# Kernel tuning notes

Hardware: AMD Instinct MI355X
Metric: run time of the kernel (lower is better)

Reference implementation:

```python
import jax, jax.numpy as jnp
import numpy as np

D = 64        # input_dim == hidden dims
D2 = 2 * D    # transformer model dim
N = 20000     # num_nodes
R = 24        # num_relation
S = 3         # history snapshots
E = 60000     # edges per snapshot
B = 8         # batch
K = 101       # candidates (1 pos + 100 neg)
HLEN = 50     # history length
NL_GNN = 2
NL_TF = 2
NH = 2        # attention heads
HD = D2 // NH


def setup_inputs() -> dict:
    key = jax.random.key(0)
    ks = list(jax.random.split(key, 40))
    nrm = lambda i, shape: jax.random.normal(ks[i], shape, jnp.float32) * 0.05
    inp = {}
    # embeddings / params
    inp["poi_emb"] = nrm(0, (N, D))
    inp["query_emb"] = nrm(1, (R, D))
    inp["gate_W"] = nrm(2, (D, D)); inp["gate_b"] = jnp.zeros((D,), jnp.float32)
    inp["gnn_rel"] = nrm(3, (NL_GNN, R, D))
    inp["gnn_W"] = nrm(4, (NL_GNN, 2 * D, D)); inp["gnn_b"] = jnp.zeros((NL_GNN, D), jnp.float32)
    inp["g_time_emb"] = nrm(5, (48, D))
    inp["g_lin_W"] = nrm(6, (D, D)); inp["g_lin_b"] = jnp.zeros((D,), jnp.float32)
    inp["tf_Wqkv"] = nrm(7, (NL_TF, D2, 3 * D2))
    inp["tf_Wo"] = nrm(8, (NL_TF, D2, D2))
    ln = jnp.stack([jnp.ones((NL_TF, D2), jnp.float32), jnp.zeros((NL_TF, D2), jnp.float32)], axis=1)
    inp["tf_ln1"] = ln; inp["tf_ln2"] = ln
    inp["tf_W1"] = nrm(9, (NL_TF, D2, 4 * D2)); inp["tf_b1"] = jnp.zeros((NL_TF, 4 * D2), jnp.float32)
    inp["tf_W2"] = nrm(10, (NL_TF, 4 * D2, D2)); inp["tf_b2"] = jnp.zeros((NL_TF, D2), jnp.float32)
    F_DIM = D + D2  # hidden_dims[-1] + 2*input_dim
    inp["mlp_W1"] = nrm(11, (F_DIM, F_DIM)); inp["mlp_b1"] = jnp.zeros((F_DIM,), jnp.float32)
    inp["mlp_W2"] = nrm(12, (F_DIM, 1)); inp["mlp_b2"] = jnp.zeros((1,), jnp.float32)
    inp["history_time_encoding"] = nrm(13, (B, HLEN, D2))
    # graph / index inputs
    inp["edge_src"] = jax.random.randint(ks[14], (S, E), 0, N)
    inp["edge_dst"] = jax.random.randint(ks[15], (S, E), 0, N)
    inp["edge_type"] = jax.random.randint(ks[16], (S, E), 0, R)
    inp["h_index"] = jax.random.randint(ks[17], (B,), 0, N)
    inp["r_index"] = jax.random.randint(ks[18], (B,), 0, R)
    inp["t_index"] = jax.random.randint(ks[19], (B, K), 0, N)
    inp["history_poi"] = jax.random.randint(ks[20], (B, HLEN), 0, N)
    inp["g_time"] = jax.random.randint(ks[21], (S,), 0, 48)
    return inp


def _layer_norm(x, scale, bias):
    m = x.mean(-1, keepdims=True)
    v = ((x - m) ** 2).mean(-1, keepdims=True)
    return (x - m) * jax.lax.rsqrt(v + 1e-5) * scale + bias


def reference(poi_emb, query_emb, gate_W, gate_b, gnn_rel, gnn_W, gnn_b,
              g_time_emb, g_lin_W, g_lin_b,
              tf_Wqkv, tf_Wo, tf_ln1, tf_W1, tf_b1, tf_W2, tf_b2, tf_ln2,
              mlp_W1, mlp_b1, mlp_W2, mlp_b2,
              history_time_encoding,
              edge_src, edge_dst, edge_type, h_index, r_index, t_index,
              history_poi, g_time):
    query = query_emb[r_index]  # [B, D]  (r_index constant across candidates)
    output = jnp.zeros((B, N, D), poi_emb.dtype)
    for s in range(S):  # temporal snapshot loop (memory_update per snapshot)
        src, dst, et = edge_src[s], edge_dst[s], edge_type[s]
        # scatter_add of poi embeddings over both endpoints; identical per batch row
        poi_node = jnp.concatenate([src, dst])  # [2E]
        init_one = jax.ops.segment_sum(poi_emb[poi_node], poi_node, num_segments=N)  # [N, D]
        init = jnp.broadcast_to(init_one[None], (B, N, D))
        if s > 0:
            gate = jax.nn.sigmoid(output @ gate_W + gate_b)  # sigmoid gating vs prior state
            init = init * gate + (1.0 - gate) * output
        x = init
        for l in range(NL_GNN):  # PathAggNet stack: transe message + scatter-sum + linear
            msg = x[:, src] + gnn_rel[l][et][None]  # [B, E, D]
            agg = jnp.zeros((B, N, D), x.dtype).at[:, dst].add(msg)  # [B, N, D]
            x = jax.nn.relu(jnp.concatenate([agg, init], axis=-1) @ gnn_W[l] + gnn_b[l])
        output = x
        query = (query + g_time_emb[g_time[s]][None]) @ g_lin_W + g_lin_b
    feature = output  # [B, N, D]
    r_emb = jnp.broadcast_to(query[:, None], (B, N, D))
    final_feature = jnp.concatenate([feature, r_emb], axis=-1)  # [B, N, 2D]
    # gather history POI features + time encoding -> transformer encoder
    poi_idx = jnp.broadcast_to(history_poi[..., None], (B, HLEN, D2))
    xseq = jnp.take_along_axis(final_feature, poi_idx, axis=1) + history_time_encoding  # [B, HLEN, 2D]
    for l in range(NL_TF):
        qkv = xseq @ tf_Wqkv[l]  # [B, HLEN, 3*D2]
        q, k, v = jnp.split(qkv, 3, axis=-1)
        split_heads = lambda t: t.reshape(B, HLEN, NH, HD).transpose(0, 2, 1, 3)
        q, k, v = split_heads(q), split_heads(k), split_heads(v)
        att = jax.nn.softmax(jnp.einsum('bnqd,bnkd->bnqk', q, k) / jnp.sqrt(jnp.float32(HD)), axis=-1)
        o = jnp.einsum('bnqk,bnkd->bnqd', att, v).transpose(0, 2, 1, 3).reshape(B, HLEN, D2) @ tf_Wo[l]
        xseq = _layer_norm(xseq + o, tf_ln1[l, 0], tf_ln1[l, 1])
        ff = jax.nn.relu(xseq @ tf_W1[l] + tf_b1[l]) @ tf_W2[l] + tf_b2[l]
        xseq = _layer_norm(xseq + ff, tf_ln2[l, 0], tf_ln2[l, 1])
    feature_label = xseq.mean(axis=1, keepdims=True)  # [B, 1, 2D]
    t_idx = jnp.broadcast_to(t_index[..., None], (B, K, D))
    feature_t = jnp.take_along_axis(feature, t_idx, axis=1)  # [B, K, D]
    feature_t = jnp.concatenate([feature_t, jnp.broadcast_to(feature_label, (B, K, D2))], axis=-1)
    hmid = jax.nn.relu(feature_t @ mlp_W1 + mlp_b1)
    score = (hmid @ mlp_W2 + mlp_b2).squeeze(-1)  # [B, K]
    return score
```

## Files before the change

### kernel.cpp

```cpp
#include <hip/hip_runtime.h>
#include <hip/hip_bf16.h>
#include <math.h>

#define DD   64
#define DD2  128
#define NN   20000
#define RR   24
#define SS   3
#define EE   60000
#define BB   8
#define KK   101
#define HLENN 50
#define MROWS 20024

__global__ void hist_kernel(const int* __restrict__ src, const int* __restrict__ dst,
                            int* __restrict__ hist, int* __restrict__ deg) {
    int s = blockIdx.y;
    int e = blockIdx.x * 256 + threadIdx.x;
    if (e < EE) {
        int d0 = dst[s * EE + e], s0 = src[s * EE + e];
        atomicAdd(&hist[s * NN + d0], 1);
        atomicAdd(&deg[s * NN + d0], 1);
        atomicAdd(&deg[s * NN + s0], 1);
    }
}

__global__ void scan_kernel(const int* __restrict__ hist, int* __restrict__ rowptr,
                            int* __restrict__ cursor) {
    int s = blockIdx.x, t = threadIdx.x;
    const int* h = hist + s * NN;
    int* rp = rowptr + s * (NN + 1);
    int* cur = cursor + s * NN;
    __shared__ int sp[1024];
    int base = t * 20, sum = 0;
    for (int i = 0; i < 20; ++i) { int idx = base + i; if (idx < NN) sum += h[idx]; }
    sp[t] = sum;
    __syncthreads();
    for (int off = 1; off < 1024; off <<= 1) {
        int v = (t >= off) ? sp[t - off] : 0;
        __syncthreads();
        sp[t] += v;
        __syncthreads();
    }
    int run = sp[t] - sum;
    for (int i = 0; i < 20; ++i) {
        int idx = base + i;
        if (idx < NN) { rp[idx] = run; cur[idx] = run; run += h[idx]; }
    }
    if (t == 1023) rp[NN] = sp[1023];
}

__global__ void place_kernel(const int* __restrict__ src, const int* __restrict__ dst,
                             const int* __restrict__ et, int* __restrict__ cursor,
                             int* __restrict__ colp) {
    int s = blockIdx.y;
    int e = blockIdx.x * 256 + threadIdx.x;
    if (e < EE) {
        int d0 = dst[s * EE + e];
        int pos = atomicAdd(&cursor[s * NN + d0], 1);
        colp[s * EE + pos] = src[s * EE + e] | (et[s * EE + e] << 16);
    }
}

__global__ void init_kernel(const float* __restrict__ poi, const int* __restrict__ deg,
                            const float* __restrict__ gate_W, const float* __restrict__ gate_b,
                            const float* __restrict__ xprev, float* __restrict__ initb,
                            int use_gate) {
    __shared__ float sW[64][64];
    __shared__ float srow[4][64];
    int li = threadIdx.x >> 6, d = threadIdx.x & 63;
    int node = blockIdx.x * 4 + li;
    if (use_gate) {
        for (int i = threadIdx.x; i < 64 * 64; i += 256) sW[i >> 6][i & 63] = gate_W[i];
    }
    float iv = (float)deg[node] * poi[node * 64 + d];
    if (use_gate) {
        float ov = xprev[node * 64 + d];
        srow[li][d] = ov;
        __syncthreads();
        float acc = gate_b[d];
        #pragma unroll
        for (int k = 0; k < 64; ++k) acc += srow[li][k] * sW[k][d];
        float g = 1.f / (1.f + expf(-acc));
        iv = iv * g + (1.f - g) * ov;
    }
    initb[node * 64 + d] = iv;
}

__global__ void gemm64_kernel(const float* __restrict__ A0a, const float* __restrict__ Ar_a,
                              const float* __restrict__ Ba, float* __restrict__ Ca,
                              const float* __restrict__ A0b, const float* __restrict__ Ar_b,
                              const float* __restrict__ Bb, float* __restrict__ Cb) {
    const float* A0 = blockIdx.y ? A0b : A0a;
    const float* Ar = blockIdx.y ? Ar_b : Ar_a;
    const float* B  = blockIdx.y ? Bb  : Ba;
    float* C        = blockIdx.y ? Cb  : Ca;
    __shared__ float sA[64][68];
    __shared__ float sB[64][68];
    int tid = threadIdx.x;
    int row0 = blockIdx.x * 64;
    for (int i = tid; i < 64 * 16; i += 256) {
        int r = i >> 4, cq = i & 15;
        int row = row0 + r;
        float4 v = make_float4(0.f, 0.f, 0.f, 0.f);
        if (row < NN)        v = *(const float4*)(A0 + (size_t)row * 64 + cq * 4);
        else if (row < MROWS) v = *(const float4*)(Ar + (size_t)(row - NN) * 64 + cq * 4);
        *(float4*)&sA[r][cq * 4] = v;
        if (i < 64 * 16) {
            float4 w = *(const float4*)(B + (size_t)r * 64 + cq * 4);
            *(float4*)&sB[r][cq * 4] = w;
        }
    }
    __syncthreads();
    int tr = tid >> 4, tc = tid & 15;
    float acc[4][4] = {{0.f}};
    #pragma unroll 16
    for (int k = 0; k < 64; ++k) {
        float4 b4 = *(const float4*)&sB[k][tc * 4];
        float a0 = sA[tr * 4 + 0][k];
        float a1 = sA[tr * 4 + 1][k];
        float a2 = sA[tr * 4 + 2][k];
        float a3 = sA[tr * 4 + 3][k];
        acc[0][0] += a0 * b4.x; acc[0][1] += a0 * b4.y; acc[0][2] += a0 * b4.z; acc[0][3] += a0 * b4.w;
        acc[1][0] += a1 * b4.x; acc[1][1] += a1 * b4.y; acc[1][2] += a1 * b4.z; acc[1][3] += a1 * b4.w;
        acc[2][0] += a2 * b4.x; acc[2][1] += a2 * b4.y; acc[2][2] += a2 * b4.z; acc[2][3] += a2 * b4.w;
        acc[3][0] += a3 * b4.x; acc[3][1] += a3 * b4.y; acc[3][2] += a3 * b4.z; acc[3][3] += a3 * b4.w;
    }
    #pragma unroll
    for (int i = 0; i < 4; ++i) {
        int row = row0 + tr * 4 + i;
        if (row < MROWS) {
            float4 o = make_float4(acc[i][0], acc[i][1], acc[i][2], acc[i][3]);
            *(float4*)(C + (size_t)row * 64 + tc * 4) = o;
        }
    }
}

__global__ void fin_kernel(const float* __restrict__ y, const float* __restrict__ z,
                           const int* __restrict__ rowptr, const int* __restrict__ colp,
                           const float* __restrict__ bias, float* __restrict__ xout) {
    __shared__ float srelW[24][64];
    int tid = threadIdx.x;
    for (int i = tid; i < 24 * 64; i += 256) srelW[i >> 6][i & 63] = y[NN * 64 + i];
    int d = tid & 63, w = tid >> 6;
    float bb = bias[d];
    __syncthreads();
    int base = blockIdx.x * 16 + w * 4;
    for (int n = 0; n < 4; ++n) {
        int node = base + n;
        float acc = z[node * 64 + d] + bb;
        int e0 = rowptr[node], e1 = rowptr[node + 1];
        for (int e = e0; e < e1; ++e) {
            int pack = colp[e];
            acc += y[(size_t)(pack & 0xFFFF) * 64 + d] + srelW[pack >> 16][d];
        }
        xout[node * 64 + d] = fmaxf(acc, 0.f);
    }
}

__global__ void query_kernel(const float* __restrict__ query_emb, const int* __restrict__ r_index,
                             const float* __restrict__ g_time_emb, const int* __restrict__ g_time,
                             const float* __restrict__ g_lin_W, const float* __restrict__ g_lin_b,
                             float* __restrict__ query) {
    __shared__ float sW[64][64];
    __shared__ float sq[8][64];
    int b = threadIdx.x >> 6;
    int d = threadIdx.x & 63;
    for (int i = threadIdx.x; i < 64 * 64; i += 512) sW[i >> 6][i & 63] = g_lin_W[i];
    float q = query_emb[r_index[b] * 64 + d];
    for (int s = 0; s < SS; ++s) {
        float t = q + g_time_emb[g_time[s] * 64 + d];
        sq[b][d] = t;
        __syncthreads();
        float acc = g_lin_b[d];
        #pragma unroll
        for (int k = 0; k < 64; ++k) acc += sq[b][k] * sW[k][d];
        q = acc;
        __syncthreads();
    }
    query[b * 64 + d] = q;
}

__global__ void xseq_kernel(const float* __restrict__ feature, const float* __restrict__ query,
                            const int* __restrict__ history_poi, const float* __restrict__ hte,
                            float* __restrict__ xseq) {
    int idx = blockIdx.x * 256 + threadIdx.x;
    if (idx >= BB * HLENN * DD2) return;
    int c = idx & 127;
    int bt = idx >> 7;
    int b = bt / HLENN, t = bt % HLENN;
    float v = (c < 64) ? feature[history_poi[b * HLENN + t] * 64 + c]
                       : query[b * 64 + (c - 64)];
    xseq[idx] = v + hte[idx];
}

__global__ void qkv4_kernel(const float* __restrict__ xseq, const float* __restrict__ Wqkv,
                            float* __restrict__ qkvb) {
    __shared__ float sx[4][128];
    int tid = threadIdx.x;
    int row0 = blockIdx.x * 4;
    for (int i = tid; i < 512; i += 384) sx[i >> 7][i & 127] = xseq[row0 * 128 + i];
    __syncthreads();
    float a0 = 0.f, a1 = 0.f, a2 = 0.f, a3 = 0.f;
    #pragma unroll 8
    for (int k = 0; k < 128; ++k) {
        float w = Wqkv[k * 384 + tid];
        a0 += sx[0][k] * w; a1 += sx[1][k] * w; a2 += sx[2][k] * w; a3 += sx[3][k] * w;
    }
    qkvb[(row0 + 0) * 384 + tid] = a0;
    qkvb[(row0 + 1) * 384 + tid] = a1;
    qkvb[(row0 + 2) * 384 + tid] = a2;
    qkvb[(row0 + 3) * 384 + tid] = a3;
}

__global__ void attn_kernel(const float* __restrict__ qkv, float* __restrict__ attnout) {
    int b = blockIdx.x >> 1, h = blockIdx.x & 1;
    __shared__ float sq[HLENN][64], sk[HLENN][64], sv[HLENN][64];
    __shared__ float ss[HLENN][HLENN];
    for (int i = threadIdx.x; i < HLENN * 64; i += 256) {
        int t = i >> 6, d = i & 63;
        const float* base = qkv + (size_t)(b * HLENN + t) * 384 + h * 64 + d;
        sq[t][d] = base[0];
        sk[t][d] = base[128];
        sv[t][d] = base[256];
    }
    __syncthreads();
    for (int p = threadIdx.x; p < HLENN * HLENN; p += 256) {
        int i = p / HLENN, j = p % HLENN;
        float acc = 0.f;
        #pragma unroll 8
        for (int d = 0; d < 64; ++d) acc += sq[i][d] * sk[j][d];
        ss[i][j] = acc * 0.125f;
    }
    __syncthreads();
    if (threadIdx.x < HLENN) {
        int i = threadIdx.x;
        float m = -1e30f;
        for (int j = 0; j < HLENN; ++j) m = fmaxf(m, ss[i][j]);
        float sum = 0.f;
        for (int j = 0; j < HLENN; ++j) { float e = expf(ss[i][j] - m); ss[i][j] = e; sum += e; }
        float inv = 1.f / sum;
        for (int j = 0; j < HLENN; ++j) ss[i][j] *= inv;
    }
    __syncthreads();
    for (int p = threadIdx.x; p < HLENN * 64; p += 256) {
        int i = p >> 6, d = p & 63;
        float acc = 0.f;
        for (int j = 0; j < HLENN; ++j) acc += ss[i][j] * sv[j][d];
        attnout[(size_t)(b * HLENN + i) * 128 + h * 64 + d] = acc;
    }
}

__global__ void addLN4_kernel(const float* __restrict__ aout, const float* __restrict__ Wo,
                              const float* __restrict__ ln, float* __restrict__ xseq) {
    __shared__ float sa[4][128];
    __shared__ float sred[4][128];
    int tid = threadIdx.x;
    int r = tid >> 7, c = tid & 127;
    int row0 = blockIdx.x * 4;
    sa[r][c] = aout[(row0 + r) * 128 + c];
    __syncthreads();
    float acc = xseq[(row0 + r) * 128 + c];
    #pragma unroll 8
    for (int k = 0; k < 128; ++k) acc += sa[r][k] * Wo[k * 128 + c];
    sred[r][c] = acc; __syncthreads();
    for (int off = 64; off > 0; off >>= 1) { if (c < off) sred[r][c] += sred[r][c + off]; __syncthreads(); }
    float mean = sred[r][0] * (1.f / 128.f);
    __syncthreads();
    float dx = acc - mean;
    sred[r][c] = dx * dx; __syncthreads();
    for (int off = 64; off > 0; off >>= 1) { if (c < off) sred[r][c] += sred[r][c + off]; __syncthreads(); }
    float var = sred[r][0] * (1.f / 128.f);
    xseq[(row0 + r) * 128 + c] = dx * rsqrtf(var + 1e-5f) * ln[c] + ln[128 + c];
}

__global__ void ffLN4_kernel(const float* __restrict__ xin, const float* __restrict__ W1,
                             const float* __restrict__ b1, const float* __restrict__ W2,
                             const float* __restrict__ b2, const float* __restrict__ ln,
                             float* __restrict__ xout) {
    __shared__ float sx[4][128];
    __shared__ float sh[4][512];
    __shared__ float spart[4][4][128];
    __shared__ float sred[4][128];
    int tid = threadIdx.x;
    int row0 = blockIdx.x * 4;
    { int r = tid >> 7, c = tid & 127; sx[r][c] = xin[(row0 + r) * 128 + c]; }
    __syncthreads();
    {
        float bb = b1[tid];
        float a0 = bb, a1 = bb, a2 = bb, a3 = bb;
        #pragma unroll 8
        for (int k = 0; k < 128; ++k) {
            float w = W1[k * 512 + tid];
            a0 += sx[0][k] * w; a1 += sx[1][k] * w; a2 += sx[2][k] * w; a3 += sx[3][k] * w;
        }
        sh[0][tid] = fmaxf(a0, 0.f); sh[1][tid] = fmaxf(a1, 0.f);
        sh[2][tid] = fmaxf(a2, 0.f); sh[3][tid] = fmaxf(a3, 0.f);
    }
    __syncthreads();
    int kc = tid >> 7, c = tid & 127;
    float p0 = 0.f, p1 = 0.f, p2 = 0.f, p3 = 0.f;
    #pragma unroll 8
    for (int kk = 0; kk < 128; ++kk) {
        int k = kc * 128 + kk;
        float w = W2[k * 128 + c];
        p0 += sh[0][k] * w; p1 += sh[1][k] * w; p2 += sh[2][k] * w; p3 += sh[3][k] * w;
    }
    spart[kc][0][c] = p0; spart[kc][1][c] = p1; spart[kc][2][c] = p2; spart[kc][3][c] = p3;
    __syncthreads();
    int r = kc;
    float acc = b2[c] + spart[0][r][c] + spart[1][r][c] + spart[2][r][c] + spart[3][r][c] + sx[r][c];
    sred[r][c] = acc; __syncthreads();
    for (int off = 64; off > 0; off >>= 1) { if (c < off) sred[r][c] += sred[r][c + off]; __syncthreads(); }
    float mean = sred[r][0] * (1.f / 128.f);
    __syncthreads();
    float dx = acc - mean;
    sred[r][c] = dx * dx; __syncthreads();
    for (int off = 64; off > 0; off >>= 1) { if (c < off) sred[r][c] += sred[r][c + off]; __syncthreads(); }
    float var = sred[r][0] * (1.f / 128.f);
    xout[(row0 + r) * 128 + c] = dx * rsqrtf(var + 1e-5f) * ln[c] + ln[128 + c];
}

__global__ void mean_kernel(const float* __restrict__ xseq, float* __restrict__ flabel) {
    int i = blockIdx.x * 256 + threadIdx.x;
    if (i >= BB * 128) return;
    int b = i >> 7, c = i & 127;
    float s = 0.f;
    for (int t = 0; t < HLENN; ++t) s += xseq[(b * HLENN + t) * 128 + c];
    flabel[i] = s * (1.f / HLENN);
}

__global__ void score_kernel(const float* __restrict__ feature, const float* __restrict__ flabel,
                             const int* __restrict__ t_index,
                             const float* __restrict__ W1, const float* __restrict__ b1,
                             const float* __restrict__ W2, const float* __restrict__ b2,
                             float* __restrict__ score) {
    int b = blockIdx.x / KK, k = blockIdx.x % KK;
    __shared__ float sf[192];
    __shared__ float sred[192];
    int j = threadIdx.x;
    int t = t_index[b * KK + k];
    sf[j] = (j < 64) ? feature[t * 64 + j] : flabel[b * 128 + (j - 64)];
    __syncthreads();
    float acc = b1[j];
    #pragma unroll 8
    for (int i = 0; i < 192; ++i) acc += sf[i] * W1[i * 192 + j];
    float h = fmaxf(acc, 0.f);
    sred[j] = h * W2[j];
    __syncthreads();
    if (j < 64) sred[j] += sred[j + 64] + sred[j + 128];
    __syncthreads();
    for (int off = 32; off > 0; off >>= 1) { if (j < off) sred[j] += sred[j + off]; __syncthreads(); }
    if (j == 0) score[b * KK + k] = sred[0] + b2[0];
}

extern "C" void kernel_launch(void* const* d_in, const int* in_sizes, int n_in,
                              void* d_out, int out_size, void* d_ws, size_t ws_size,
                              hipStream_t stream) {
    const float* poi_emb   = (const float*)d_in[0];
    const float* query_emb = (const float*)d_in[1];
    const float* gate_W    = (const float*)d_in[2];
    const float* gate_b    = (const float*)d_in[3];
    const float* gnn_rel   = (const float*)d_in[4];
    const float* gnn_W     = (const float*)d_in[5];
    const float* gnn_b     = (const float*)d_in[6];
    const float* g_time_emb= (const float*)d_in[7];
    const float* g_lin_W   = (const float*)d_in[8];
    const float* g_lin_b   = (const float*)d_in[9];
    const float* tf_Wqkv   = (const float*)d_in[10];
    const float* tf_Wo     = (const float*)d_in[11];
    const float* tf_ln1    = (const float*)d_in[12];
    const float* tf_ln2    = (const float*)d_in[13];
    const float* tf_W1     = (const float*)d_in[14];
    const float* tf_b1     = (const float*)d_in[15];
    const float* tf_W2     = (const float*)d_in[16];
    const float* tf_b2     = (const float*)d_in[17];
    const float* mlp_W1    = (const float*)d_in[18];
    const float* mlp_b1    = (const float*)d_in[19];
    const float* mlp_W2    = (const float*)d_in[20];
    const float* mlp_b2    = (const float*)d_in[21];
    const float* hte       = (const float*)d_in[22];
    const int* edge_src    = (const int*)d_in[23];
    const int* edge_dst    = (const int*)d_in[24];
    const int* edge_type   = (const int*)d_in[25];
    const int* r_index     = (const int*)d_in[27];
    const int* t_index     = (const int*)d_in[28];
    const int* history_poi = (const int*)d_in[29];
    const int* g_time      = (const int*)d_in[30];

    float* ws = (float*)d_ws;
    float* xA    = ws;
    float* xB    = xA + 1280000;
    float* initb = xB + 1280000;
    float* y     = initb + 1280000;
    float* z     = y + 20032 * 64;
    float* query = z + 20032 * 64;
    float* xseq  = query + 512;
    float* qkvb  = xseq + 51200;
    float* aout  = qkvb + 153600;
    float* flab  = aout + 51200;
    int* hist    = (int*)(flab + 1024);
    int* deg     = hist + 3 * NN;
    int* rowptr  = deg + 3 * NN;
    int* cursor  = rowptr + 3 * (NN + 1);
    int* colp    = cursor + 3 * NN;

    hipMemsetAsync(hist, 0, 2 * 3 * NN * sizeof(int), stream);
    {
        dim3 g((EE + 255) / 256, 3);
        hist_kernel<<<g, 256, 0, stream>>>(edge_src, edge_dst, hist, deg);
        scan_kernel<<<3, 1024, 0, stream>>>(hist, rowptr, cursor);
        place_kernel<<<g, 256, 0, stream>>>(edge_src, edge_dst, edge_type, cursor, colp);
    }

    for (int s = 0; s < SS; ++s) {
        const int* rp = rowptr + s * (NN + 1);
        const int* cp = colp + s * EE;
        init_kernel<<<NN / 4, 256, 0, stream>>>(poi_emb, deg + s * NN, gate_W, gate_b,
                                                xA, initb, s > 0 ? 1 : 0);
        const float* Wt0 = gnn_W;
        const float* Wb0 = gnn_W + 64 * 64;
        const float* Wt1 = gnn_W + 128 * 64;
        const float* Wb1 = gnn_W + 128 * 64 + 64 * 64;
        const float* rel0 = gnn_rel;
        const float* rel1 = gnn_rel + 24 * 64;
        dim3 gg(313, 2);
        gemm64_kernel<<<gg, 256, 0, stream>>>(initb, rel0, Wt0, y,
                                              initb, rel0, Wb0, z);
        fin_kernel<<<NN / 16, 256, 0, stream>>>(y, z, rp, cp, gnn_b, xB);
        gemm64_kernel<<<gg, 256, 0, stream>>>(xB, rel1, Wt1, y,
                                              initb, rel1, Wb1, z);
        fin_kernel<<<NN / 16, 256, 0, stream>>>(y, z, rp, cp, gnn_b + 64, xA);
    }

    query_kernel<<<1, 512, 0, stream>>>(query_emb, r_index, g_time_emb, g_time,
                                        g_lin_W, g_lin_b, query);
    xseq_kernel<<<(BB * HLENN * 128 + 255) / 256, 256, 0, stream>>>(xA, query, history_poi, hte, xseq);

    for (int l = 0; l < 2; ++l) {
        qkv4_kernel<<<BB * HLENN / 4, 384, 0, stream>>>(xseq, tf_Wqkv + l * 128 * 384, qkvb);
        attn_kernel<<<BB * 2, 256, 0, stream>>>(qkvb, aout);
        addLN4_kernel<<<BB * HLENN / 4, 512, 0, stream>>>(aout, tf_Wo + l * 128 * 128,
                                                          tf_ln1 + l * 256, xseq);
        ffLN4_kernel<<<BB * HLENN / 4, 512, 0, stream>>>(xseq, tf_W1 + l * 128 * 512,
                                                         tf_b1 + l * 512, tf_W2 + l * 512 * 128,
                                                         tf_b2 + l * 128, tf_ln2 + l * 256, xseq);
    }

    mean_kernel<<<(BB * 128 + 255) / 256, 256, 0, stream>>>(xseq, flab);
    score_kernel<<<BB * KK, 192, 0, stream>>>(xA, flab, t_index,
                                              mlp_W1, mlp_b1, mlp_W2, mlp_b2, (float*)d_out);
}
```

Measured before the change: 526.0 us.

## Fuse CSR build into one LDS kernel and fuse GNN init/gather with GEMMs

Replaces the memset plus hist/scan/place kernels with a single per-snapshot kernel that builds the CSR and degree arrays using shared-memory atomics. It also fuses the gated init into the first layer's dual GEMM, and the layer-1 gather/ReLU into the layer-2 dual GEMM. This cuts per-snapshot launches from five to three and avoids round-tripping intermediate node features through global memory. The trade-offs are that CSR construction now runs on only 3 blocks, and the fused kernels use more LDS with less parallelism per phase.

```diff
diff --git a/kernel.cpp b/kernel.cpp
--- a/kernel.cpp
+++ b/kernel.cpp
@@ -13,27 +13,25 @@
 #define HLENN 50
 #define MROWS 20024
 
-__global__ void hist_kernel(const int* __restrict__ src, const int* __restrict__ dst,
-                            int* __restrict__ hist, int* __restrict__ deg) {
-    int s = blockIdx.y;
-    int e = blockIdx.x * 256 + threadIdx.x;
-    if (e < EE) {
-        int d0 = dst[s * EE + e], s0 = src[s * EE + e];
-        atomicAdd(&hist[s * NN + d0], 1);
-        atomicAdd(&deg[s * NN + d0], 1);
-        atomicAdd(&deg[s * NN + s0], 1);
-    }
-}
-
-__global__ void scan_kernel(const int* __restrict__ hist, int* __restrict__ rowptr,
-                            int* __restrict__ cursor) {
+__global__ __launch_bounds__(1024) void csr_kernel(
+        const int* __restrict__ src, const int* __restrict__ dst,
+        const int* __restrict__ et,
+        int* __restrict__ rowptr,
+        int* __restrict__ colp,
+        int* __restrict__ deg) {
+    __shared__ int lh[NN];
+    __shared__ int sp[1024];
     int s = blockIdx.x, t = threadIdx.x;
-    const int* h = hist + s * NN;
+    const int* ps = src + s * EE;
+    const int* pd = dst + s * EE;
+    const int* pt = et + s * EE;
     int* rp = rowptr + s * (NN + 1);
-    int* cur = cursor + s * NN;
-    __shared__ int sp[1024];
+    for (int i = t; i < NN; i += 1024) lh[i] = 0;
+    __syncthreads();
+    for (int e = t; e < EE; e += 1024) atomicAdd(&lh[pd[e]], 1);
+    __syncthreads();
     int base = t * 20, sum = 0;
-    for (int i = 0; i < 20; ++i) { int idx = base + i; if (idx < NN) sum += h[idx]; }
+    for (int i = 0; i < 20; ++i) { int idx = base + i; if (idx < NN) sum += lh[idx]; }
     sp[t] = sum;
     __syncthreads();
     for (int off = 1; off < 1024; off <<= 1) {
@@ -45,116 +43,183 @@
     int run = sp[t] - sum;
     for (int i = 0; i < 20; ++i) {
         int idx = base + i;
-        if (idx < NN) { rp[idx] = run; cur[idx] = run; run += h[idx]; }
+        if (idx < NN) { rp[idx] = run; int c = lh[idx]; lh[idx] = run; run += c; }
     }
     if (t == 1023) rp[NN] = sp[1023];
-}
-
-__global__ void place_kernel(const int* __restrict__ src, const int* __restrict__ dst,
-                             const int* __restrict__ et, int* __restrict__ cursor,
-                             int* __restrict__ colp) {
-    int s = blockIdx.y;
-    int e = blockIdx.x * 256 + threadIdx.x;
-    if (e < EE) {
-        int d0 = dst[s * EE + e];
-        int pos = atomicAdd(&cursor[s * NN + d0], 1);
-        colp[s * EE + pos] = src[s * EE + e] | (et[s * EE + e] << 16);
-    }
-}
-
-__global__ void init_kernel(const float* __restrict__ poi, const int* __restrict__ deg,
-                            const float* __restrict__ gate_W, const float* __restrict__ gate_b,
-                            const float* __restrict__ xprev, float* __restrict__ initb,
-                            int use_gate) {
-    __shared__ float sW[64][64];
+    __syncthreads();
+    for (int e = t; e < EE; e += 1024) {
+        int pos = atomicAdd(&lh[pd[e]], 1);
+        colp[s * EE + pos] = ps[e] | (pt[e] << 16);
+    }
+    __syncthreads();
+    for (int i = t; i < NN; i += 1024) lh[i] = 0;
+    __syncthreads();
+    for (int e = t; e < EE; e += 1024) atomicAdd(&lh[ps[e]], 1);
+    __syncthreads();
+    for (int i = t; i < NN; i += 1024)
+        deg[s * NN + i] = lh[i] + (rp[i + 1] - rp[i]);
+}
+
+__global__ __launch_bounds__(256) void initgemm_kernel(
+        const float* __restrict__ poi, const int* __restrict__ deg,
+        const float* __restrict__ gate_W, const float* __restrict__ gate_b,
+        const float* __restrict__ xprev, const float* __restrict__ rel,
+        const float* __restrict__ W,
+        float* __restrict__ initb, float* __restrict__ y, float* __restrict__ z,
+        int use_gate) {
+    __shared__ float sGW[64][64];
+    __shared__ float sA[64][68];
+    __shared__ float sBt[64][68];
+    __shared__ float sBb[64][68];
     __shared__ float srow[4][64];
-    int li = threadIdx.x >> 6, d = threadIdx.x & 63;
-    int node = blockIdx.x * 4 + li;
+    int tid = threadIdx.x;
+    int li = tid >> 6, d = tid & 63;
+    int row0 = blockIdx.x * 64;
     if (use_gate) {
-        for (int i = threadIdx.x; i < 64 * 64; i += 256) sW[i >> 6][i & 63] = gate_W[i];
-    }
-    float iv = (float)deg[node] * poi[node * 64 + d];
-    if (use_gate) {
-        float ov = xprev[node * 64 + d];
-        srow[li][d] = ov;
+        for (int i = tid; i < 64 * 64; i += 256) sGW[i >> 6][i & 63] = gate_W[i];
         __syncthreads();
-        float acc = gate_b[d];
+    }
+    float gb = use_gate ? gate_b[d] : 0.f;
+    for (int it = 0; it < 16; ++it) {
+        int rl = it * 4 + li;
+        int row = row0 + rl;
+        float iv;
+        if (row < NN)           iv = (float)deg[row] * poi[(size_t)row * 64 + d];
+        else if (row < MROWS)   iv = rel[(row - NN) * 64 + d];
+        else                    iv = 0.f;
+        if (use_gate) {
+            float ov = (row < NN) ? xprev[(size_t)row * 64 + d] : 0.f;
+            srow[li][d] = ov;
+            __syncthreads();
+            float acc = gb;
+            #pragma unroll
+            for (int k = 0; k < 64; ++k) acc += srow[li][k] * sGW[k][d];
+            float g = 1.f / (1.f + expf(-acc));
+            if (row < NN) iv = iv * g + (1.f - g) * ov;
+            __syncthreads();
+        }
+        sA[rl][d] = iv;
+        if (row < NN) initb[(size_t)row * 64 + d] = iv;
+    }
+    for (int i = tid; i < 64 * 64; i += 256) {
+        sBt[i >> 6][i & 63] = W[i];
+        sBb[i >> 6][i & 63] = W[64 * 64 + i];
+    }
+    __syncthreads();
+    int tr = tid >> 4, tc = tid & 15;
+    float accY[4][4] = {{0.f}}, accZ[4][4] = {{0.f}};
+    #pragma unroll 16
+    for (int k = 0; k < 64; ++k) {
+        float4 bt = *(const float4*)&sBt[k][tc * 4];
+        float4 bz = *(const float4*)&sBb[k][tc * 4];
         #pragma unroll
-        for (int k = 0; k < 64; ++k) acc += srow[li][k] * sW[k][d];
-        float g = 1.f / (1.f + expf(-acc));
-        iv = iv * g + (1.f - g) * ov;
-    }
-    initb[node * 64 + d] = iv;
-}
-
-__global__ void gemm64_kernel(const float* __restrict__ A0a, const float* __restrict__ Ar_a,
-                              const float* __restrict__ Ba, float* __restrict__ Ca,
-                              const float* __restrict__ A0b, const float* __restrict__ Ar_b,
-                              const float* __restrict__ Bb, float* __restrict__ Cb) {
-    const float* A0 = blockIdx.y ? A0b : A0a;
-    const float* Ar = blockIdx.y ? Ar_b : Ar_a;
-    const float* B  = blockIdx.y ? Bb  : Ba;
-    float* C        = blockIdx.y ? Cb  : Ca;
+        for (int i = 0; i < 4; ++i) {
+            float a = sA[tr * 4 + i][k];
+            accY[i][0] += a * bt.x; accY[i][1] += a * bt.y; accY[i][2] += a * bt.z; accY[i][3] += a * bt.w;
+            accZ[i][0] += a * bz.x; accZ[i][1] += a * bz.y; accZ[i][2] += a * bz.z; accZ[i][3] += a * bz.w;
+        }
+    }
+    #pragma unroll
+    for (int i = 0; i < 4; ++i) {
+        int row = row0 + tr * 4 + i;
+        if (row < MROWS) {
+            *(float4*)(y + (size_t)row * 64 + tc * 4) = make_float4(accY[i][0], accY[i][1], accY[i][2], accY[i][3]);
+            *(float4*)(z + (size_t)row * 64 + tc * 4) = make_float4(accZ[i][0], accZ[i][1], accZ[i][2], accZ[i][3]);
+        }
+    }
+}
+
+__global__ __launch_bounds__(256) void fingemm_kernel(
+        const float* __restrict__ y, const float* __restrict__ z,
+        const int* __restrict__ rp, const int* __restrict__ cp,
+        const float* __restrict__ bias0, const float* __restrict__ rel1,
+        const float* __restrict__ W1,
+        const float* __restrict__ initb,
+        float* __restrict__ y2, float* __restrict__ z2) {
+    __shared__ float srelW[24][64];
     __shared__ float sA[64][68];
-    __shared__ float sB[64][68];
+    __shared__ float sAi[64][68];
+    __shared__ float sBt[64][68];
+    __shared__ float sBb[64][68];
     int tid = threadIdx.x;
+    int li = tid >> 6, d = tid & 63;
     int row0 = blockIdx.x * 64;
+    for (int i = tid; i < 24 * 64; i += 256) srelW[i >> 6][i & 63] = y[(size_t)NN * 64 + i];
+    for (int i = tid; i < 64 * 64; i += 256) {
+        sBt[i >> 6][i & 63] = W1[i];
+        sBb[i >> 6][i & 63] = W1[64 * 64 + i];
+    }
     for (int i = tid; i < 64 * 16; i += 256) {
         int r = i >> 4, cq = i & 15;
         int row = row0 + r;
         float4 v = make_float4(0.f, 0.f, 0.f, 0.f);
-        if (row < NN)        v = *(const float4*)(A0 + (size_t)row * 64 + cq * 4);
-        else if (row < MROWS) v = *(const float4*)(Ar + (size_t)(row - NN) * 64 + cq * 4);
-        *(float4*)&sA[r][cq * 4] = v;
-        if (i < 64 * 16) {
-            float4 w = *(const float4*)(B + (size_t)r * 64 + cq * 4);
-            *(float4*)&sB[r][cq * 4] = w;
-        }
+        if (row < NN) v = *(const float4*)(initb + (size_t)row * 64 + cq * 4);
+        *(float4*)&sAi[r][cq * 4] = v;
+    }
+    __syncthreads();
+    float bb0 = bias0[d];
+    for (int it = 0; it < 16; ++it) {
+        int rl = it * 4 + li;
+        int row = row0 + rl;
+        float val = 0.f;
+        if (row < NN) {
+            float acc = z[(size_t)row * 64 + d] + bb0;
+            int e0 = rp[row], e1 = rp[row + 1];
+            for (int e = e0; e < e1; ++e) {
+                int pack = cp[e];
+                acc += y[(size_t)(pack & 0xFFFF) * 64 + d] + srelW[pack >> 16][d];
+            }
+            val = fmaxf(acc, 0.f);
+        } else if (row < MROWS) {
+            val = rel1[(row - NN) * 64 + d];
+        }
+        sA[rl][d] = val;
     }
     __syncthreads();
     int tr = tid >> 4, tc = tid & 15;
-    float acc[4][4] = {{0.f}};
+    float accY[4][4] = {{0.f}}, accZ[4][4] = {{0.f}};
     #pragma unroll 16
     for (int k = 0; k < 64; ++k) {
-        float4 b4 = *(const float4*)&sB[k][tc * 4];
-        float a0 = sA[tr * 4 + 0][k];
-        float a1 = sA[tr * 4 + 1][k];
-        float a2 = sA[tr * 4 + 2][k];
-        float a3 = sA[tr * 4 + 3][k];
-        acc[0][0] += a0 * b4.x; acc[0][1] += a0 * b4.y; acc[0][2] += a0 * b4.z; acc[0][3] += a0 * b4.w;
-        acc[1][0] += a1 * b4.x; acc[1][1] += a1 * b4.y; acc[1][2] += a1 * b4.z; acc[1][3] += a1 * b4.w;
-        acc[2][0] += a2 * b4.x; acc[2][1] += a2 * b4.y; acc[2][2] += a2 * b4.z; acc[2][3] += a2 * b4.w;
-        acc[3][0] += a3 * b4.x; acc[3][1] += a3 * b4.y; acc[3][2] += a3 * b4.z; acc[3][3] += a3 * b4.w;
+        float4 bt = *(const float4*)&sBt[k][tc * 4];
+        float4 bz = *(const float4*)&sBb[k][tc * 4];
+        #pragma unroll
+        for (int i = 0; i < 4; ++i) {
+            float a  = sA[tr * 4 + i][k];
+            float ai = sAi[tr * 4 + i][k];
+            accY[i][0] += a * bt.x;  accY[i][1] += a * bt.y;  accY[i][2] += a * bt.z;  accY[i][3] += a * bt.w;
+            accZ[i][0] += ai * bz.x; accZ[i][1] += ai * bz.y; accZ[i][2] += ai * bz.z; accZ[i][3] += ai * bz.w;
+        }
     }
     #pragma unroll
     for (int i = 0; i < 4; ++i) {
         int row = row0 + tr * 4 + i;
         if (row < MROWS) {
-            float4 o = make_float4(acc[i][0], acc[i][1], acc[i][2], acc[i][3]);
-            *(float4*)(C + (size_t)row * 64 + tc * 4) = o;
-        }
-    }
-}
-
-__global__ void fin_kernel(const float* __restrict__ y, const float* __restrict__ z,
-                           const int* __restrict__ rowptr, const int* __restrict__ colp,
-                           const float* __restrict__ bias, float* __restrict__ xout) {
+            *(float4*)(y2 + (size_t)row * 64 + tc * 4) = make_float4(accY[i][0], accY[i][1], accY[i][2], accY[i][3]);
+            *(float4*)(z2 + (size_t)row * 64 + tc * 4) = make_float4(accZ[i][0], accZ[i][1], accZ[i][2], accZ[i][3]);
+        }
+    }
+}
+
+__global__ __launch_bounds__(256) void fin_kernel(
+        const float* __restrict__ y, const float* __restrict__ z,
+        const int* __restrict__ rowptr, const int* __restrict__ colp,
+        const float* __restrict__ bias, float* __restrict__ xout) {
     __shared__ float srelW[24][64];
     int tid = threadIdx.x;
-    for (int i = tid; i < 24 * 64; i += 256) srelW[i >> 6][i & 63] = y[NN * 64 + i];
+    for (int i = tid; i < 24 * 64; i += 256) srelW[i >> 6][i & 63] = y[(size_t)NN * 64 + i];
     int d = tid & 63, w = tid >> 6;
     float bb = bias[d];
     __syncthreads();
     int base = blockIdx.x * 16 + w * 4;
     for (int n = 0; n < 4; ++n) {
         int node = base + n;
-        float acc = z[node * 64 + d] + bb;
+        float acc = z[(size_t)node * 64 + d] + bb;
         int e0 = rowptr[node], e1 = rowptr[node + 1];
         for (int e = e0; e < e1; ++e) {
             int pack = colp[e];
             acc += y[(size_t)(pack & 0xFFFF) * 64 + d] + srelW[pack >> 16][d];
         }
-        xout[node * 64 + d] = fmaxf(acc, 0.f);
+        xout[(size_t)node * 64 + d] = fmaxf(acc, 0.f);
     }
 }
 
@@ -189,7 +254,7 @@
     int c = idx & 127;
     int bt = idx >> 7;
     int b = bt / HLENN, t = bt % HLENN;
-    float v = (c < 64) ? feature[history_poi[b * HLENN + t] * 64 + c]
+    float v = (c < 64) ? feature[(size_t)history_poi[b * HLENN + t] * 64 + c]
                        : query[b * 64 + (c - 64)];
     xseq[idx] = v + hte[idx];
 }
@@ -330,17 +395,18 @@
     flabel[i] = s * (1.f / HLENN);
 }
 
-__global__ void score_kernel(const float* __restrict__ feature, const float* __restrict__ flabel,
-                             const int* __restrict__ t_index,
-                             const float* __restrict__ W1, const float* __restrict__ b1,
-                             const float* __restrict__ W2, const float* __restrict__ b2,
-                             float* __restrict__ score) {
+__global__ __launch_bounds__(192) void score_kernel(
+        const float* __restrict__ feature, const float* __restrict__ flabel,
+        const int* __restrict__ t_index,
+        const float* __restrict__ W1, const float* __restrict__ b1,
+        const float* __restrict__ W2, const float* __restrict__ b2,
+        float* __restrict__ score) {
     int b = blockIdx.x / KK, k = blockIdx.x % KK;
     __shared__ float sf[192];
     __shared__ float sred[192];
     int j = threadIdx.x;
     int t = t_index[b * KK + k];
-    sf[j] = (j < 64) ? feature[t * 64 + j] : flabel[b * 128 + (j - 64)];
+    sf[j] = (j < 64) ? feature[(size_t)t * 64 + j] : flabel[b * 128 + (j - 64)];
     __syncthreads();
     float acc = b1[j];
     #pragma unroll 8
@@ -390,47 +456,33 @@
 
     float* ws = (float*)d_ws;
     float* xA    = ws;
-    float* xB    = xA + 1280000;
-    float* initb = xB + 1280000;
+    float* initb = xA    + 1280000;
     float* y     = initb + 1280000;
-    float* z     = y + 20032 * 64;
-    float* query = z + 20032 * 64;
+    float* z     = y     + 1282048;
+    float* y2    = z     + 1282048;
+    float* z2    = y2    + 1282048;
+    float* query = z2    + 1282048;
     float* xseq  = query + 512;
-    float* qkvb  = xseq + 51200;
-    float* aout  = qkvb + 153600;
-    float* flab  = aout + 51200;
-    int* hist    = (int*)(flab + 1024);
-    int* deg     = hist + 3 * NN;
-    int* rowptr  = deg + 3 * NN;
-    int* cursor  = rowptr + 3 * (NN + 1);
-    int* colp    = cursor + 3 * NN;
-
-    hipMemsetAsync(hist, 0, 2 * 3 * NN * sizeof(int), stream);
-    {
-        dim3 g((EE + 255) / 256, 3);
-        hist_kernel<<<g, 256, 0, stream>>>(edge_src, edge_dst, hist, deg);
-        scan_kernel<<<3, 1024, 0, stream>>>(hist, rowptr, cursor);
-        place_kernel<<<g, 256, 0, stream>>>(edge_src, edge_dst, edge_type, cursor, colp);
-    }
+    float* qkvb  = xseq  + 51200;
+    float* aout  = qkvb  + 153600;
+    float* flab  = aout  + 51200;
+    int* rowptr  = (int*)(flab + 1024);
+    int* colp    = rowptr + 3 * (NN + 1);
+    int* deg     = colp + 3 * EE;
+
+    csr_kernel<<<3, 1024, 0, stream>>>(edge_src, edge_dst, edge_type,
+                                       rowptr, colp, deg);
 
     for (int s = 0; s < SS; ++s) {
         const int* rp = rowptr + s * (NN + 1);
         const int* cp = colp + s * EE;
-        init_kernel<<<NN / 4, 256, 0, stream>>>(poi_emb, deg + s * NN, gate_W, gate_b,
-                                                xA, initb, s > 0 ? 1 : 0);
-        const float* Wt0 = gnn_W;
-        const float* Wb0 = gnn_W + 64 * 64;
-        const float* Wt1 = gnn_W + 128 * 64;
-        const float* Wb1 = gnn_W + 128 * 64 + 64 * 64;
-        const float* rel0 = gnn_rel;
-        const float* rel1 = gnn_rel + 24 * 64;
-        dim3 gg(313, 2);
-        gemm64_kernel<<<gg, 256, 0, stream>>>(initb, rel0, Wt0, y,
-                                              initb, rel0, Wb0, z);
-        fin_kernel<<<NN / 16, 256, 0, stream>>>(y, z, rp, cp, gnn_b, xB);
-        gemm64_kernel<<<gg, 256, 0, stream>>>(xB, rel1, Wt1, y,
-                                              initb, rel1, Wb1, z);
-        fin_kernel<<<NN / 16, 256, 0, stream>>>(y, z, rp, cp, gnn_b + 64, xA);
+        initgemm_kernel<<<313, 256, 0, stream>>>(
+            poi_emb, deg + s * NN, gate_W, gate_b, xA,
+            gnn_rel, gnn_W, initb, y, z, s > 0 ? 1 : 0);
+        fingemm_kernel<<<313, 256, 0, stream>>>(
+            y, z, rp, cp, gnn_b,
+            gnn_rel + 24 * 64, gnn_W + 128 * 64, initb, y2, z2);
+        fin_kernel<<<NN / 16, 256, 0, stream>>>(y2, z2, rp, cp, gnn_b + 64, xA);
     }
 
     query_kernel<<<1, 512, 0, stream>>>(query_emb, r_index, g_time_emb, g_time,
```

After: 713.4 us. 35.6% more time.
